# Kernel tuning notes

Hardware: AMD Instinct MI355X
Metric: run time of the kernel (lower is better)

The kernel has to match this reference:

```python
import jax, jax.numpy as jnp
import numpy as np


def setup_inputs() -> dict:
    key = jax.random.key(0)
    kq, kk, kv = jax.random.split(key, 3)
    B, T, D = 8, 4096, 64
    q = jax.random.normal(kq, (B, T, D), dtype=jnp.float32)
    k = jax.random.normal(kk, (B, T, D), dtype=jnp.float32)
    v = jax.random.normal(kv, (B, T, D), dtype=jnp.float32)
    return {"q": q, "k": k, "v": v}


def reference(q, k, v):
    # q,k,v: [b, t, d]
    b, t_q, d = q.shape
    t_k = k.shape[1]
    scale = 1.0 / jnp.sqrt(jnp.asarray(d, dtype=q.dtype))
    qk = jnp.einsum('bqd,bkd->bqk', q, k) * scale  # [b, t_q, t_k]
    # causal mask: positions t2 > t1 set to -inf (replaces the Python double-loop)
    causal_mask = jnp.arange(t_k)[None, :] > jnp.arange(t_q)[:, None]  # [t_q, t_k]
    qk = jnp.where(causal_mask[None, :, :], -jnp.inf, qk)
    attn = jax.nn.softmax(qk, axis=-1)
    return jnp.einsum('bqk,bkd->bqd', attn, v)
```

## Files before the change

### kernel.cpp

```cpp
#include <hip/hip_runtime.h>

namespace {

constexpr float QSC = 0.18033688f;

typedef short bf16x8 __attribute__((ext_vector_type(8)));
typedef float f32x4 __attribute__((ext_vector_type(4)));

typedef __attribute__((address_space(3))) unsigned int lds_u32;
typedef __attribute__((address_space(1))) const unsigned int gbl_u32;

__device__ inline float exp2x(float x) { return __builtin_amdgcn_exp2f(x); }

__device__ inline unsigned int pack2(float a, float b) {
  unsigned int ua = __builtin_bit_cast(unsigned int, a);
  unsigned int ub = __builtin_bit_cast(unsigned int, b);
  ua = (ua + 0x8000u) >> 16;
  ub = (ub + 0x8000u) & 0xFFFF0000u;
  return ua | ub;
}

__device__ inline void gl_lds16(const unsigned short* g, unsigned short* l) {
  __builtin_amdgcn_global_load_lds((gbl_u32*)g, (lds_u32*)l, 16, 0, 0);
}

__device__ inline bf16x8 ld16(const unsigned short* p) {
  uint4 u = *(const uint4*)p;
  return __builtin_bit_cast(bf16x8, u);
}

__global__ __launch_bounds__(256) void prep(const float* __restrict__ K,
                                            const float* __restrict__ V,
                                            unsigned short* __restrict__ Kbf,
                                            unsigned short* __restrict__ Vtb) {
  __shared__ float Vl[64 * 65];
  const int bid = blockIdx.x;
  const int b = bid >> 6, kt = bid & 63;
  const int tid = threadIdx.x;
  const float4* Ks4 = (const float4*)(K + ((size_t)b * 4096 + kt * 64) * 64);
  const float4* Vs4 = (const float4*)(V + ((size_t)b * 4096 + kt * 64) * 64);
  #pragma unroll
  for (int i = 0; i < 4; ++i) {
    int idx = tid + 256 * i;
    int row = idx >> 4, c4 = idx & 15;
    float4 t = Ks4[idx];
    *(uint2*)&Kbf[((size_t)b * 4096 + kt * 64 + row) * 64 + c4 * 4] =
        make_uint2(pack2(t.x, t.y), pack2(t.z, t.w));
    float4 tv = Vs4[idx];
    float* d = &Vl[row * 65 + c4 * 4];
    d[0] = tv.x; d[1] = tv.y; d[2] = tv.z; d[3] = tv.w;
  }
  __syncthreads();
  #pragma unroll
  for (int i = 0; i < 4; ++i) {
    int idx = tid + 256 * i;
    int dd = idx >> 4, kc = idx & 15;
    float a  = Vl[(kc * 4 + 0) * 65 + dd];
    float b2 = Vl[(kc * 4 + 1) * 65 + dd];
    float c  = Vl[(kc * 4 + 2) * 65 + dd];
    float e  = Vl[(kc * 4 + 3) * 65 + dd];
    *(uint2*)&Vtb[((size_t)b * 64 + dd) * 4096 + kt * 64 + kc * 4] =
        make_uint2(pack2(a, b2), pack2(c, e));
  }
}

__launch_bounds__(512, 4)
__global__ void fa_mfma(const float* __restrict__ Q,
                        float* __restrict__ O,
                        const unsigned short* __restrict__ Kbf,
                        const unsigned short* __restrict__ Vtb) {
  __shared__ __align__(16) unsigned short smem[32768];

  const int bid = blockIdx.x;
  int b, qt;
  if (bid < 256) { b = bid & 7; qt = bid >> 3; }
  else           { b = bid & 7; qt = 63 - ((bid - 256) >> 3); }

  const int tid  = threadIdx.x;
  const int w    = tid >> 6;
  const int g    = w >> 2;
  const int wg   = w & 3;
  const int lane = tid & 63;
  const int quad = lane >> 4;
  const int lc   = lane & 15;

  unsigned short* Kb0 = &smem[(g * 2 + 0) * 4096];
  unsigned short* Kb1 = &smem[(g * 2 + 1) * 4096];
  unsigned short* Vb  = &smem[16384 + g * 4096];
  unsigned short* Pl  = &smem[24576 + w * 1024];

  const unsigned short* Kt_g = Kbf + (size_t)b * 4096 * 64;
  const unsigned short* Vt_g = Vtb + (size_t)b * 64 * 4096;

  const int r0 = wg * 16 + (lane >> 3);
  const int c0 = (lane & 7) ^ (r0 & 7);

  const int ph0 = (quad ^ (lc & 7)) * 8;
  const int ph1 = ((4 + quad) ^ (lc & 7)) * 8;

  const size_t base = (size_t)b * 4096 * 64;
  const float* Qb = Q + base + (size_t)qt * 64 * 64;
  float* Ob = O + base + (size_t)qt * 64 * 64;

  bf16x8 qf[2];
  {
    const float* qrow = Qb + (wg * 16 + lc) * 64 + quad * 8;
    #pragma unroll
    for (int ks = 0; ks < 2; ++ks) {
      float4 x = *(const float4*)(qrow + ks * 32);
      float4 y = *(const float4*)(qrow + ks * 32 + 4);
      uint4 u = make_uint4(pack2(x.x * QSC, x.y * QSC), pack2(x.z * QSC, x.w * QSC),
                           pack2(y.x * QSC, y.y * QSC), pack2(y.z * QSC, y.w * QSC));
      qf[ks] = __builtin_bit_cast(bf16x8, u);
    }
  }

  if (g <= qt) {
    const unsigned short* gk = Kt_g + (size_t)(g * 64) * 64;
    gl_lds16(gk + (size_t)r0 * 64 + c0 * 8, Kb0 + wg * 1024);
    gl_lds16(gk + (size_t)(r0 + 8) * 64 + c0 * 8, Kb0 + wg * 1024 + 512);
  }

  float l_i = 0.0f;
  f32x4 o[4];
  #pragma unroll
  for (int nt = 0; nt < 4; ++nt) o[nt] = f32x4{0.f, 0.f, 0.f, 0.f};

  const int nIter = qt / 2 + 1;
  for (int i = 0; i < nIter; ++i) {
    const int kt = 2 * i + g;
    const bool active = (kt <= qt);
    unsigned short* Kcur = (i & 1) ? Kb1 : Kb0;
    unsigned short* Knxt = (i & 1) ? Kb0 : Kb1;

    __syncthreads();

    if (active) {
      const unsigned short* gv = Vt_g + kt * 64;
      gl_lds16(gv + (size_t)r0 * 4096 + c0 * 8, Vb + wg * 1024);
      gl_lds16(gv + (size_t)(r0 + 8) * 4096 + c0 * 8, Vb + wg * 1024 + 512);
    }
    if (kt + 2 <= qt) {
      const unsigned short* gk = Kt_g + (size_t)((kt + 2) * 64) * 64;
      gl_lds16(gk + (size_t)r0 * 64 + c0 * 8, Knxt + wg * 1024);
      gl_lds16(gk + (size_t)(r0 + 8) * 64 + c0 * 8, Knxt + wg * 1024 + 512);
    }

    if (active) {
      f32x4 st[4];
      #pragma unroll
      for (int t = 0; t < 4; ++t) {
        f32x4 c = {0.f, 0.f, 0.f, 0.f};
        c = __builtin_amdgcn_mfma_f32_16x16x32_bf16(ld16(&Kcur[(t * 16 + lc) * 64 + ph0]), qf[0], c, 0, 0, 0);
        c = __builtin_amdgcn_mfma_f32_16x16x32_bf16(ld16(&Kcur[(t * 16 + lc) * 64 + ph1]), qf[1], c, 0, 0, 0);
        st[t] = c;
      }

      const bool diag = (kt == qt);
      const int qrow = wg * 16 + lc;
      #pragma unroll
      for (int t = 0; t < 4; ++t) {
        float e[4];
        #pragma unroll
        for (int r = 0; r < 4; ++r) {
          int key_l = 16 * t + quad * 4 + r;
          float v = st[t][r];
          if (diag && key_l > qrow) v = -1e30f;
          e[r] = exp2x(v);
        }
        l_i += (e[0] + e[1]) + (e[2] + e[3]);
        *(uint2*)&Pl[lc * 64 + ((2 * t + (quad >> 1)) ^ (lc & 7)) * 8 + (quad & 1) * 4] =
            make_uint2(pack2(e[0], e[1]), pack2(e[2], e[3]));
      }
    }

    __syncthreads();

    if (active) {
      #pragma unroll
      for (int ks = 0; ks < 2; ++ks) {
        bf16x8 a = ld16(&Pl[lc * 64 + (ks ? ph1 : ph0)]);
        #pragma unroll
        for (int nt = 0; nt < 4; ++nt) {
          bf16x8 bfr = ld16(&Vb[(nt * 16 + lc) * 64 + (ks ? ph1 : ph0)]);
          o[nt] = __builtin_amdgcn_mfma_f32_16x16x32_bf16(a, bfr, o[nt], 0, 0, 0);
        }
      }
    }
  }

  l_i += __shfl_xor(l_i, 16);
  l_i += __shfl_xor(l_i, 32);

  constexpr int MSTR = 66;
  float* mrg = (float*)smem;
  if (g == 1) {
    #pragma unroll
    for (int r = 0; r < 4; ++r) {
      int row = wg * 16 + quad * 4 + r;
      #pragma unroll
      for (int nt = 0; nt < 4; ++nt)
        mrg[row * MSTR + nt * 16 + lc] = o[nt][r];
    }
    if (quad == 0)
      mrg[64 * MSTR + wg * 16 + lc] = l_i;
  }
  __syncthreads();
  if (g == 0) {
    const int row0 = wg * 16 + lc;
    float linv = 1.0f / (l_i + mrg[64 * MSTR + row0]);
    float lv[4];
    #pragma unroll
    for (int r = 0; r < 4; ++r) lv[r] = __shfl(linv, quad * 4 + r);
    #pragma unroll
    for (int r = 0; r < 4; ++r) {
      int row = wg * 16 + quad * 4 + r;
      float* orow = Ob + row * 64 + lc;
      #pragma unroll
      for (int nt = 0; nt < 4; ++nt) {
        float o1 = mrg[row * MSTR + nt * 16 + lc];
        orow[nt * 16] = (o[nt][r] + o1) * lv[r];
      }
    }
  }
}

}

extern "C" void kernel_launch(void* const* d_in, const int* in_sizes, int n_in,
                              void* d_out, int out_size, void* d_ws, size_t ws_size,
                              hipStream_t stream) {
  const float* q = (const float*)d_in[0];
  const float* k = (const float*)d_in[1];
  const float* v = (const float*)d_in[2];
  float* out = (float*)d_out;
  unsigned short* Kbf = (unsigned short*)d_ws;
  unsigned short* Vtb = Kbf + (size_t)8 * 4096 * 64;
  prep<<<dim3(512), dim3(256), 0, stream>>>(k, v, Kbf, Vtb);
  fa_mfma<<<dim3(512), dim3(512), 0, stream>>>(q, out, Kbf, Vtb);
}
```

Before: 121.0 us.

## Split KV halves across separate blocks with atomic-flag cross-block merge

Each query tile's two key-parity halves now run in separate 256-thread blocks (1024 blocks total) instead of two wave groups inside one 512-thread block. Partial outputs and row sums go to a global workspace, and the last-arriving block, found through an atomic counter, merges and normalizes them. The diagonal-mask branch is also split out so non-diagonal tiles skip the mask compare. The aim is finer scheduling granularity and lower per-block LDS, at the cost of extra global traffic, fences, and a bf16-rounded partial for the g=1 half.

Result: slower. 292.3 us (+141.6%).

```diff
diff --git a/kernel.cpp b/kernel.cpp
--- a/kernel.cpp
+++ b/kernel.cpp
@@ -20,6 +20,16 @@
   return ua | ub;
 }
 
+__device__ inline float bf2f(unsigned short u) {
+  unsigned int v = (unsigned int)u << 16;
+  return __builtin_bit_cast(float, v);
+}
+
+__device__ inline unsigned short f2bf(float a) {
+  unsigned int ua = __builtin_bit_cast(unsigned int, a);
+  return (unsigned short)((ua + 0x8000u) >> 16);
+}
+
 __device__ inline void gl_lds16(const unsigned short* g, unsigned short* l) {
   __builtin_amdgcn_global_load_lds((gbl_u32*)g, (lds_u32*)l, 16, 0, 0);
 }
@@ -32,11 +42,13 @@
 __global__ __launch_bounds__(256) void prep(const float* __restrict__ K,
                                             const float* __restrict__ V,
                                             unsigned short* __restrict__ Kbf,
-                                            unsigned short* __restrict__ Vtb) {
+                                            unsigned short* __restrict__ Vtb,
+                                            int* __restrict__ flags) {
   __shared__ float Vl[64 * 65];
   const int bid = blockIdx.x;
   const int b = bid >> 6, kt = bid & 63;
   const int tid = threadIdx.x;
+  if (tid == 0) flags[bid] = 0;
   const float4* Ks4 = (const float4*)(K + ((size_t)b * 4096 + kt * 64) * 64);
   const float4* Vs4 = (const float4*)(V + ((size_t)b * 4096 + kt * 64) * 64);
   #pragma unroll
@@ -64,35 +76,38 @@
   }
 }
 
-__launch_bounds__(512, 4)
+__launch_bounds__(256, 4)
 __global__ void fa_mfma(const float* __restrict__ Q,
                         float* __restrict__ O,
                         const unsigned short* __restrict__ Kbf,
-                        const unsigned short* __restrict__ Vtb) {
-  __shared__ __align__(16) unsigned short smem[32768];
+                        const unsigned short* __restrict__ Vtb,
+                        unsigned short* __restrict__ wsP,
+                        float* __restrict__ wsl,
+                        int* __restrict__ flags) {
+  __shared__ __align__(16) unsigned short smem[16384];
+  __shared__ int bcast;
 
   const int bid = blockIdx.x;
-  int b, qt;
-  if (bid < 256) { b = bid & 7; qt = bid >> 3; }
-  else           { b = bid & 7; qt = 63 - ((bid - 256) >> 3); }
+  const int j = bid & 255, s = bid >> 8;
+  const int b = j >> 5, a = j & 31;
+  const int qt = (s & 2) ? (63 - a) : a;
+  const int g = s & 1;
 
   const int tid  = threadIdx.x;
   const int w    = tid >> 6;
-  const int g    = w >> 2;
-  const int wg   = w & 3;
   const int lane = tid & 63;
   const int quad = lane >> 4;
   const int lc   = lane & 15;
 
-  unsigned short* Kb0 = &smem[(g * 2 + 0) * 4096];
-  unsigned short* Kb1 = &smem[(g * 2 + 1) * 4096];
-  unsigned short* Vb  = &smem[16384 + g * 4096];
-  unsigned short* Pl  = &smem[24576 + w * 1024];
+  unsigned short* Kb0 = &smem[0];
+  unsigned short* Kb1 = &smem[4096];
+  unsigned short* Vb  = &smem[8192];
+  unsigned short* Pl  = &smem[12288 + w * 1024];
 
   const unsigned short* Kt_g = Kbf + (size_t)b * 4096 * 64;
   const unsigned short* Vt_g = Vtb + (size_t)b * 64 * 4096;
 
-  const int r0 = wg * 16 + (lane >> 3);
+  const int r0 = w * 16 + (lane >> 3);
   const int c0 = (lane & 7) ^ (r0 & 7);
 
   const int ph0 = (quad ^ (lc & 7)) * 8;
@@ -101,10 +116,11 @@
   const size_t base = (size_t)b * 4096 * 64;
   const float* Qb = Q + base + (size_t)qt * 64 * 64;
   float* Ob = O + base + (size_t)qt * 64 * 64;
+  const int slot = b * 64 + qt;
 
   bf16x8 qf[2];
   {
-    const float* qrow = Qb + (wg * 16 + lc) * 64 + quad * 8;
+    const float* qrow = Qb + (w * 16 + lc) * 64 + quad * 8;
     #pragma unroll
     for (int ks = 0; ks < 2; ++ks) {
       float4 x = *(const float4*)(qrow + ks * 32);
@@ -117,8 +133,8 @@
 
   if (g <= qt) {
     const unsigned short* gk = Kt_g + (size_t)(g * 64) * 64;
-    gl_lds16(gk + (size_t)r0 * 64 + c0 * 8, Kb0 + wg * 1024);
-    gl_lds16(gk + (size_t)(r0 + 8) * 64 + c0 * 8, Kb0 + wg * 1024 + 512);
+    gl_lds16(gk + (size_t)r0 * 64 + c0 * 8, Kb0 + w * 1024);
+    gl_lds16(gk + (size_t)(r0 + 8) * 64 + c0 * 8, Kb0 + w * 1024 + 512);
   }
 
   float l_i = 0.0f;
@@ -137,13 +153,13 @@
 
     if (active) {
       const unsigned short* gv = Vt_g + kt * 64;
-      gl_lds16(gv + (size_t)r0 * 4096 + c0 * 8, Vb + wg * 1024);
-      gl_lds16(gv + (size_t)(r0 + 8) * 4096 + c0 * 8, Vb + wg * 1024 + 512);
+      gl_lds16(gv + (size_t)r0 * 4096 + c0 * 8, Vb + w * 1024);
+      gl_lds16(gv + (size_t)(r0 + 8) * 4096 + c0 * 8, Vb + w * 1024 + 512);
     }
     if (kt + 2 <= qt) {
       const unsigned short* gk = Kt_g + (size_t)((kt + 2) * 64) * 64;
-      gl_lds16(gk + (size_t)r0 * 64 + c0 * 8, Knxt + wg * 1024);
-      gl_lds16(gk + (size_t)(r0 + 8) * 64 + c0 * 8, Knxt + wg * 1024 + 512);
+      gl_lds16(gk + (size_t)r0 * 64 + c0 * 8, Knxt + w * 1024);
+      gl_lds16(gk + (size_t)(r0 + 8) * 64 + c0 * 8, Knxt + w * 1024 + 512);
     }
 
     if (active) {
@@ -156,21 +172,30 @@
         st[t] = c;
       }
 
-      const bool diag = (kt == qt);
-      const int qrow = wg * 16 + lc;
-      #pragma unroll
-      for (int t = 0; t < 4; ++t) {
-        float e[4];
+      if (kt == qt) {
+        const int qrow = w * 16 + lc;
         #pragma unroll
-        for (int r = 0; r < 4; ++r) {
-          int key_l = 16 * t + quad * 4 + r;
-          float v = st[t][r];
-          if (diag && key_l > qrow) v = -1e30f;
-          e[r] = exp2x(v);
+        for (int t = 0; t < 4; ++t) {
+          float e[4];
+          #pragma unroll
+          for (int r = 0; r < 4; ++r) {
+            int key_l = 16 * t + quad * 4 + r;
+            e[r] = (key_l > qrow) ? 0.0f : exp2x(st[t][r]);
+          }
+          l_i += (e[0] + e[1]) + (e[2] + e[3]);
+          *(uint2*)&Pl[lc * 64 + ((2 * t + (quad >> 1)) ^ (lc & 7)) * 8 + (quad & 1) * 4] =
+              make_uint2(pack2(e[0], e[1]), pack2(e[2], e[3]));
         }
-        l_i += (e[0] + e[1]) + (e[2] + e[3]);
-        *(uint2*)&Pl[lc * 64 + ((2 * t + (quad >> 1)) ^ (lc & 7)) * 8 + (quad & 1) * 4] =
-            make_uint2(pack2(e[0], e[1]), pack2(e[2], e[3]));
+      } else {
+        #pragma unroll
+        for (int t = 0; t < 4; ++t) {
+          float e[4];
+          #pragma unroll
+          for (int r = 0; r < 4; ++r) e[r] = exp2x(st[t][r]);
+          l_i += (e[0] + e[1]) + (e[2] + e[3]);
+          *(uint2*)&Pl[lc * 64 + ((2 * t + (quad >> 1)) ^ (lc & 7)) * 8 + (quad & 1) * 4] =
+              make_uint2(pack2(e[0], e[1]), pack2(e[2], e[3]));
+        }
       }
     }
 
@@ -179,11 +204,11 @@
     if (active) {
       #pragma unroll
       for (int ks = 0; ks < 2; ++ks) {
-        bf16x8 a = ld16(&Pl[lc * 64 + (ks ? ph1 : ph0)]);
+        bf16x8 pa = ld16(&Pl[lc * 64 + (ks ? ph1 : ph0)]);
         #pragma unroll
         for (int nt = 0; nt < 4; ++nt) {
           bf16x8 bfr = ld16(&Vb[(nt * 16 + lc) * 64 + (ks ? ph1 : ph0)]);
-          o[nt] = __builtin_amdgcn_mfma_f32_16x16x32_bf16(a, bfr, o[nt], 0, 0, 0);
+          o[nt] = __builtin_amdgcn_mfma_f32_16x16x32_bf16(pa, bfr, o[nt], 0, 0, 0);
         }
       }
     }
@@ -192,34 +217,41 @@
   l_i += __shfl_xor(l_i, 16);
   l_i += __shfl_xor(l_i, 32);
 
-  constexpr int MSTR = 66;
-  float* mrg = (float*)smem;
-  if (g == 1) {
+  if (g == 0) {
     #pragma unroll
     for (int r = 0; r < 4; ++r) {
-      int row = wg * 16 + quad * 4 + r;
-      #pragma unroll
-      for (int nt = 0; nt < 4; ++nt)
-        mrg[row * MSTR + nt * 16 + lc] = o[nt][r];
-    }
-    if (quad == 0)
-      mrg[64 * MSTR + wg * 16 + lc] = l_i;
-  }
+      int row = w * 16 + quad * 4 + r;
+      float* orow = Ob + row * 64 + lc;
+      #pragma unroll
+      for (int nt = 0; nt < 4; ++nt) orow[nt * 16] = o[nt][r];
+    }
+  } else {
+    unsigned short* ps = wsP + (size_t)slot * 4096;
+    #pragma unroll
+    for (int r = 0; r < 4; ++r) {
+      int row = w * 16 + quad * 4 + r;
+      #pragma unroll
+      for (int nt = 0; nt < 4; ++nt) ps[row * 64 + nt * 16 + lc] = f2bf(o[nt][r]);
+    }
+  }
+  if (quad == 0) wsl[slot * 128 + g * 64 + w * 16 + lc] = l_i;
+
+  __threadfence();
   __syncthreads();
-  if (g == 0) {
-    const int row0 = wg * 16 + lc;
-    float linv = 1.0f / (l_i + mrg[64 * MSTR + row0]);
-    float lv[4];
-    #pragma unroll
-    for (int r = 0; r < 4; ++r) lv[r] = __shfl(linv, quad * 4 + r);
+  if (tid == 0) bcast = atomicAdd(&flags[slot], 1);
+  __syncthreads();
+  if (bcast == 1) {
+    __threadfence();
+    const unsigned short* ps = wsP + (size_t)slot * 4096;
     #pragma unroll
     for (int r = 0; r < 4; ++r) {
-      int row = wg * 16 + quad * 4 + r;
+      int row = w * 16 + quad * 4 + r;
+      float linv = 1.0f / (wsl[slot * 128 + row] + wsl[slot * 128 + 64 + row]);
       float* orow = Ob + row * 64 + lc;
       #pragma unroll
       for (int nt = 0; nt < 4; ++nt) {
-        float o1 = mrg[row * MSTR + nt * 16 + lc];
-        orow[nt * 16] = (o[nt][r] + o1) * lv[r];
+        float sib = (g == 0) ? bf2f(ps[row * 64 + nt * 16 + lc]) : orow[nt * 16];
+        orow[nt * 16] = (o[nt][r] + sib) * linv;
       }
     }
   }
@@ -236,6 +268,9 @@
   float* out = (float*)d_out;
   unsigned short* Kbf = (unsigned short*)d_ws;
   unsigned short* Vtb = Kbf + (size_t)8 * 4096 * 64;
-  prep<<<dim3(512), dim3(256), 0, stream>>>(k, v, Kbf, Vtb);
-  fa_mfma<<<dim3(512), dim3(512), 0, stream>>>(q, out, Kbf, Vtb);
-}
+  unsigned short* wsP = Vtb + (size_t)8 * 4096 * 64;
+  float* wsl = (float*)(wsP + (size_t)512 * 4096);
+  int* flags = (int*)(wsl + (size_t)512 * 128);
+  prep<<<dim3(512), dim3(256), 0, stream>>>(k, v, Kbf, Vtb, flags);
+  fa_mfma<<<dim3(1024), dim3(256), 0, stream>>>(q, out, Kbf, Vtb, wsP, wsl, flags);
+}
```

## Load K and V fragments straight from global into registers, drop LDS staging

Applied to the files above, without the earlier changes.

Removes the double-buffered LDS staging of K and V tiles (global_load_lds) and the per-iteration block-wide barriers. Each wave now reads its MFMA operand fragments for K and transposed V directly from global memory into registers, and the masked diagonal tile gets its own softmax branch. This shrinks shared memory to the per-wave P scratch plus the merge area, which needs one barrier before the final merge. The cost is redundant global/L2 reads: the four waves in a group each fetch the same tiles. Load latency is also no longer hidden by a prefetch.

New measurement: 191.7 us. +58.5%, slower.

```diff
diff --git a/kernel.cpp b/kernel.cpp
--- a/kernel.cpp
+++ b/kernel.cpp
@@ -6,9 +6,6 @@
 
 typedef short bf16x8 __attribute__((ext_vector_type(8)));
 typedef float f32x4 __attribute__((ext_vector_type(4)));
-
-typedef __attribute__((address_space(3))) unsigned int lds_u32;
-typedef __attribute__((address_space(1))) const unsigned int gbl_u32;
 
 __device__ inline float exp2x(float x) { return __builtin_amdgcn_exp2f(x); }
 
@@ -18,10 +15,6 @@
   ua = (ua + 0x8000u) >> 16;
   ub = (ub + 0x8000u) & 0xFFFF0000u;
   return ua | ub;
-}
-
-__device__ inline void gl_lds16(const unsigned short* g, unsigned short* l) {
-  __builtin_amdgcn_global_load_lds((gbl_u32*)g, (lds_u32*)l, 16, 0, 0);
 }
 
 __device__ inline bf16x8 ld16(const unsigned short* p) {
@@ -69,7 +62,7 @@
                         float* __restrict__ O,
                         const unsigned short* __restrict__ Kbf,
                         const unsigned short* __restrict__ Vtb) {
-  __shared__ __align__(16) unsigned short smem[32768];
+  __shared__ __align__(16) unsigned short smem[8704];
 
   const int bid = blockIdx.x;
   int b, qt;
@@ -84,16 +77,10 @@
   const int quad = lane >> 4;
   const int lc   = lane & 15;
 
-  unsigned short* Kb0 = &smem[(g * 2 + 0) * 4096];
-  unsigned short* Kb1 = &smem[(g * 2 + 1) * 4096];
-  unsigned short* Vb  = &smem[16384 + g * 4096];
-  unsigned short* Pl  = &smem[24576 + w * 1024];
+  unsigned short* Pl = &smem[w * 1024];
 
   const unsigned short* Kt_g = Kbf + (size_t)b * 4096 * 64;
   const unsigned short* Vt_g = Vtb + (size_t)b * 64 * 4096;
-
-  const int r0 = wg * 16 + (lane >> 3);
-  const int c0 = (lane & 7) ^ (r0 & 7);
 
   const int ph0 = (quad ^ (lc & 7)) * 8;
   const int ph1 = ((4 + quad) ^ (lc & 7)) * 8;
@@ -115,48 +102,33 @@
     }
   }
 
-  if (g <= qt) {
-    const unsigned short* gk = Kt_g + (size_t)(g * 64) * 64;
-    gl_lds16(gk + (size_t)r0 * 64 + c0 * 8, Kb0 + wg * 1024);
-    gl_lds16(gk + (size_t)(r0 + 8) * 64 + c0 * 8, Kb0 + wg * 1024 + 512);
-  }
-
   float l_i = 0.0f;
   f32x4 o[4];
   #pragma unroll
   for (int nt = 0; nt < 4; ++nt) o[nt] = f32x4{0.f, 0.f, 0.f, 0.f};
 
-  const int nIter = qt / 2 + 1;
-  for (int i = 0; i < nIter; ++i) {
-    const int kt = 2 * i + g;
-    const bool active = (kt <= qt);
-    unsigned short* Kcur = (i & 1) ? Kb1 : Kb0;
-    unsigned short* Knxt = (i & 1) ? Kb0 : Kb1;
-
-    __syncthreads();
-
-    if (active) {
-      const unsigned short* gv = Vt_g + kt * 64;
-      gl_lds16(gv + (size_t)r0 * 4096 + c0 * 8, Vb + wg * 1024);
-      gl_lds16(gv + (size_t)(r0 + 8) * 4096 + c0 * 8, Vb + wg * 1024 + 512);
-    }
-    if (kt + 2 <= qt) {
-      const unsigned short* gk = Kt_g + (size_t)((kt + 2) * 64) * 64;
-      gl_lds16(gk + (size_t)r0 * 64 + c0 * 8, Knxt + wg * 1024);
-      gl_lds16(gk + (size_t)(r0 + 8) * 64 + c0 * 8, Knxt + wg * 1024 + 512);
-    }
-
-    if (active) {
-      f32x4 st[4];
-      #pragma unroll
-      for (int t = 0; t < 4; ++t) {
-        f32x4 c = {0.f, 0.f, 0.f, 0.f};
-        c = __builtin_amdgcn_mfma_f32_16x16x32_bf16(ld16(&Kcur[(t * 16 + lc) * 64 + ph0]), qf[0], c, 0, 0, 0);
-        c = __builtin_amdgcn_mfma_f32_16x16x32_bf16(ld16(&Kcur[(t * 16 + lc) * 64 + ph1]), qf[1], c, 0, 0, 0);
-        st[t] = c;
-      }
-
-      const bool diag = (kt == qt);
+  for (int kt = g; kt <= qt; kt += 2) {
+    const unsigned short* kb = Kt_g + (size_t)kt * 64 * 64;
+    f32x4 st[4];
+    #pragma unroll
+    for (int t = 0; t < 4; ++t) {
+      bf16x8 a0 = ld16(kb + (t * 16 + lc) * 64 + quad * 8);
+      bf16x8 a1 = ld16(kb + (t * 16 + lc) * 64 + 32 + quad * 8);
+      f32x4 c = {0.f, 0.f, 0.f, 0.f};
+      c = __builtin_amdgcn_mfma_f32_16x16x32_bf16(a0, qf[0], c, 0, 0, 0);
+      c = __builtin_amdgcn_mfma_f32_16x16x32_bf16(a1, qf[1], c, 0, 0, 0);
+      st[t] = c;
+    }
+
+    bf16x8 vf[4][2];
+    const unsigned short* vb = Vt_g + kt * 64;
+    #pragma unroll
+    for (int nt = 0; nt < 4; ++nt) {
+      vf[nt][0] = ld16(vb + (size_t)(nt * 16 + lc) * 4096 + quad * 8);
+      vf[nt][1] = ld16(vb + (size_t)(nt * 16 + lc) * 4096 + 32 + quad * 8);
+    }
+
+    if (kt == qt) {
       const int qrow = wg * 16 + lc;
       #pragma unroll
       for (int t = 0; t < 4; ++t) {
@@ -164,27 +136,31 @@
         #pragma unroll
         for (int r = 0; r < 4; ++r) {
           int key_l = 16 * t + quad * 4 + r;
-          float v = st[t][r];
-          if (diag && key_l > qrow) v = -1e30f;
-          e[r] = exp2x(v);
+          e[r] = (key_l > qrow) ? 0.0f : exp2x(st[t][r]);
         }
         l_i += (e[0] + e[1]) + (e[2] + e[3]);
         *(uint2*)&Pl[lc * 64 + ((2 * t + (quad >> 1)) ^ (lc & 7)) * 8 + (quad & 1) * 4] =
             make_uint2(pack2(e[0], e[1]), pack2(e[2], e[3]));
       }
-    }
-
-    __syncthreads();
-
-    if (active) {
-      #pragma unroll
-      for (int ks = 0; ks < 2; ++ks) {
-        bf16x8 a = ld16(&Pl[lc * 64 + (ks ? ph1 : ph0)]);
+    } else {
+      #pragma unroll
+      for (int t = 0; t < 4; ++t) {
+        float e[4];
         #pragma unroll
-        for (int nt = 0; nt < 4; ++nt) {
-          bf16x8 bfr = ld16(&Vb[(nt * 16 + lc) * 64 + (ks ? ph1 : ph0)]);
-          o[nt] = __builtin_amdgcn_mfma_f32_16x16x32_bf16(a, bfr, o[nt], 0, 0, 0);
-        }
+        for (int r = 0; r < 4; ++r) e[r] = exp2x(st[t][r]);
+        l_i += (e[0] + e[1]) + (e[2] + e[3]);
+        *(uint2*)&Pl[lc * 64 + ((2 * t + (quad >> 1)) ^ (lc & 7)) * 8 + (quad & 1) * 4] =
+            make_uint2(pack2(e[0], e[1]), pack2(e[2], e[3]));
+      }
+    }
+
+    {
+      bf16x8 pa0 = ld16(&Pl[lc * 64 + ph0]);
+      bf16x8 pa1 = ld16(&Pl[lc * 64 + ph1]);
+      #pragma unroll
+      for (int nt = 0; nt < 4; ++nt) {
+        o[nt] = __builtin_amdgcn_mfma_f32_16x16x32_bf16(pa0, vf[nt][0], o[nt], 0, 0, 0);
+        o[nt] = __builtin_amdgcn_mfma_f32_16x16x32_bf16(pa1, vf[nt][1], o[nt], 0, 0, 0);
       }
     }
   }
@@ -194,6 +170,7 @@
 
   constexpr int MSTR = 66;
   float* mrg = (float*)smem;
+  __syncthreads();
   if (g == 1) {
     #pragma unroll
     for (int r = 0; r < 4; ++r) {
```

## Split key and D halves across waves, read V fragments directly from global

Applied to the files above, without the earlier changes.

Reworks how work inside each 64x64 tile is split across the four waves of a group. Each wave now covers a 32-query by 32-key by 32-dim slice instead of 16 full query rows. The P tile is shared per group in LDS instead of being held per wave. V fragments are loaded straight from global into registers rather than staged through LDS, which shrinks LDS use and may raise occupancy. The cost is four partial accumulators that must be reduced through a serialized LDS merge with extra barriers, plus global-latency V loads inside the loop.

After: 121.2 us. About the same (+0.2%).

```diff
diff --git a/kernel.cpp b/kernel.cpp
--- a/kernel.cpp
+++ b/kernel.cpp
@@ -69,7 +69,7 @@
                         float* __restrict__ O,
                         const unsigned short* __restrict__ Kbf,
                         const unsigned short* __restrict__ Vtb) {
-  __shared__ __align__(16) unsigned short smem[32768];
+  __shared__ __align__(16) unsigned short smem[24576];
 
   const int bid = blockIdx.x;
   int b, qt;
@@ -80,14 +80,15 @@
   const int w    = tid >> 6;
   const int g    = w >> 2;
   const int wg   = w & 3;
+  const int kh   = wg & 1;
+  const int h2   = wg >> 1;
   const int lane = tid & 63;
   const int quad = lane >> 4;
   const int lc   = lane & 15;
 
   unsigned short* Kb0 = &smem[(g * 2 + 0) * 4096];
   unsigned short* Kb1 = &smem[(g * 2 + 1) * 4096];
-  unsigned short* Vb  = &smem[16384 + g * 4096];
-  unsigned short* Pl  = &smem[24576 + w * 1024];
+  unsigned short* Pg  = &smem[16384 + g * 4096];
 
   const unsigned short* Kt_g = Kbf + (size_t)b * 4096 * 64;
   const unsigned short* Vt_g = Vtb + (size_t)b * 64 * 4096;
@@ -95,23 +96,23 @@
   const int r0 = wg * 16 + (lane >> 3);
   const int c0 = (lane & 7) ^ (r0 & 7);
 
-  const int ph0 = (quad ^ (lc & 7)) * 8;
-  const int ph1 = ((4 + quad) ^ (lc & 7)) * 8;
+  const int lx = lc & 7;
 
   const size_t base = (size_t)b * 4096 * 64;
   const float* Qb = Q + base + (size_t)qt * 64 * 64;
   float* Ob = O + base + (size_t)qt * 64 * 64;
 
-  bf16x8 qf[2];
-  {
-    const float* qrow = Qb + (wg * 16 + lc) * 64 + quad * 8;
+  bf16x8 qf[2][2];
+  #pragma unroll
+  for (int q2 = 0; q2 < 2; ++q2) {
+    const float* qrow = Qb + (h2 * 32 + q2 * 16 + lc) * 64 + quad * 8;
     #pragma unroll
     for (int ks = 0; ks < 2; ++ks) {
       float4 x = *(const float4*)(qrow + ks * 32);
       float4 y = *(const float4*)(qrow + ks * 32 + 4);
       uint4 u = make_uint4(pack2(x.x * QSC, x.y * QSC), pack2(x.z * QSC, x.w * QSC),
                            pack2(y.x * QSC, y.y * QSC), pack2(y.z * QSC, y.w * QSC));
-      qf[ks] = __builtin_bit_cast(bf16x8, u);
+      qf[q2][ks] = __builtin_bit_cast(bf16x8, u);
     }
   }
 
@@ -121,10 +122,12 @@
     gl_lds16(gk + (size_t)(r0 + 8) * 64 + c0 * 8, Kb0 + wg * 1024 + 512);
   }
 
-  float l_i = 0.0f;
-  f32x4 o[4];
-  #pragma unroll
-  for (int nt = 0; nt < 4; ++nt) o[nt] = f32x4{0.f, 0.f, 0.f, 0.f};
+  float l_p[2] = {0.f, 0.f};
+  f32x4 o[4][2];
+  #pragma unroll
+  for (int m = 0; m < 4; ++m)
+    #pragma unroll
+    for (int n = 0; n < 2; ++n) o[m][n] = f32x4{0.f, 0.f, 0.f, 0.f};
 
   const int nIter = qt / 2 + 1;
   for (int i = 0; i < nIter; ++i) {
@@ -135,42 +138,50 @@
 
     __syncthreads();
 
-    if (active) {
-      const unsigned short* gv = Vt_g + kt * 64;
-      gl_lds16(gv + (size_t)r0 * 4096 + c0 * 8, Vb + wg * 1024);
-      gl_lds16(gv + (size_t)(r0 + 8) * 4096 + c0 * 8, Vb + wg * 1024 + 512);
-    }
     if (kt + 2 <= qt) {
       const unsigned short* gk = Kt_g + (size_t)((kt + 2) * 64) * 64;
       gl_lds16(gk + (size_t)r0 * 64 + c0 * 8, Knxt + wg * 1024);
       gl_lds16(gk + (size_t)(r0 + 8) * 64 + c0 * 8, Knxt + wg * 1024 + 512);
     }
 
+    bf16x8 vf[2];
     if (active) {
-      f32x4 st[4];
-      #pragma unroll
-      for (int t = 0; t < 4; ++t) {
-        f32x4 c = {0.f, 0.f, 0.f, 0.f};
-        c = __builtin_amdgcn_mfma_f32_16x16x32_bf16(ld16(&Kcur[(t * 16 + lc) * 64 + ph0]), qf[0], c, 0, 0, 0);
-        c = __builtin_amdgcn_mfma_f32_16x16x32_bf16(ld16(&Kcur[(t * 16 + lc) * 64 + ph1]), qf[1], c, 0, 0, 0);
-        st[t] = c;
+      #pragma unroll
+      for (int n = 0; n < 2; ++n)
+        vf[n] = ld16(Vt_g + (size_t)(h2 * 32 + n * 16 + lc) * 4096 + kt * 64 + kh * 32 + quad * 8);
+
+      f32x4 st[2][2];
+      #pragma unroll
+      for (int k2 = 0; k2 < 2; ++k2) {
+        const int arow = kh * 32 + k2 * 16 + lc;
+        bf16x8 a0 = ld16(Kcur + arow * 64 + (quad ^ lx) * 8);
+        bf16x8 a1 = ld16(Kcur + arow * 64 + ((4 + quad) ^ lx) * 8);
+        #pragma unroll
+        for (int q2 = 0; q2 < 2; ++q2) {
+          f32x4 c = {0.f, 0.f, 0.f, 0.f};
+          c = __builtin_amdgcn_mfma_f32_16x16x32_bf16(a0, qf[q2][0], c, 0, 0, 0);
+          c = __builtin_amdgcn_mfma_f32_16x16x32_bf16(a1, qf[q2][1], c, 0, 0, 0);
+          st[q2][k2] = c;
+        }
       }
 
       const bool diag = (kt == qt);
-      const int qrow = wg * 16 + lc;
-      #pragma unroll
-      for (int t = 0; t < 4; ++t) {
-        float e[4];
-        #pragma unroll
-        for (int r = 0; r < 4; ++r) {
-          int key_l = 16 * t + quad * 4 + r;
-          float v = st[t][r];
-          if (diag && key_l > qrow) v = -1e30f;
-          e[r] = exp2x(v);
-        }
-        l_i += (e[0] + e[1]) + (e[2] + e[3]);
-        *(uint2*)&Pl[lc * 64 + ((2 * t + (quad >> 1)) ^ (lc & 7)) * 8 + (quad & 1) * 4] =
-            make_uint2(pack2(e[0], e[1]), pack2(e[2], e[3]));
+      #pragma unroll
+      for (int q2 = 0; q2 < 2; ++q2) {
+        const int qrow_l = h2 * 32 + q2 * 16 + lc;
+        #pragma unroll
+        for (int k2 = 0; k2 < 2; ++k2) {
+          float e[4];
+          #pragma unroll
+          for (int r = 0; r < 4; ++r) {
+            int key_l = kh * 32 + k2 * 16 + quad * 4 + r;
+            float v = st[q2][k2][r];
+            e[r] = (diag && key_l > qrow_l) ? 0.0f : exp2x(v);
+          }
+          l_p[q2] += (e[0] + e[1]) + (e[2] + e[3]);
+          *(uint2*)&Pg[qrow_l * 64 + ((kh * 4 + k2 * 2 + (quad >> 1)) ^ lx) * 8 + (quad & 1) * 4] =
+              make_uint2(pack2(e[0], e[1]), pack2(e[2], e[3]));
+        }
       }
     }
 
@@ -178,50 +189,66 @@
 
     if (active) {
       #pragma unroll
-      for (int ks = 0; ks < 2; ++ks) {
-        bf16x8 a = ld16(&Pl[lc * 64 + (ks ? ph1 : ph0)]);
-        #pragma unroll
-        for (int nt = 0; nt < 4; ++nt) {
-          bf16x8 bfr = ld16(&Vb[(nt * 16 + lc) * 64 + (ks ? ph1 : ph0)]);
-          o[nt] = __builtin_amdgcn_mfma_f32_16x16x32_bf16(a, bfr, o[nt], 0, 0, 0);
-        }
-      }
-    }
-  }
-
-  l_i += __shfl_xor(l_i, 16);
-  l_i += __shfl_xor(l_i, 32);
-
-  constexpr int MSTR = 66;
+      for (int m = 0; m < 4; ++m) {
+        bf16x8 pa = ld16(&Pg[(m * 16 + lc) * 64 + ((kh * 4 + quad) ^ lx) * 8]);
+        #pragma unroll
+        for (int n = 0; n < 2; ++n)
+          o[m][n] = __builtin_amdgcn_mfma_f32_16x16x32_bf16(pa, vf[n], o[m][n], 0, 0, 0);
+      }
+    }
+  }
+
+  #pragma unroll
+  for (int q2 = 0; q2 < 2; ++q2) {
+    l_p[q2] += __shfl_xor(l_p[q2], 16);
+    l_p[q2] += __shfl_xor(l_p[q2], 32);
+  }
+
   float* mrg = (float*)smem;
-  if (g == 1) {
-    #pragma unroll
-    for (int r = 0; r < 4; ++r) {
-      int row = wg * 16 + quad * 4 + r;
-      #pragma unroll
-      for (int nt = 0; nt < 4; ++nt)
-        mrg[row * MSTR + nt * 16 + lc] = o[nt][r];
-    }
-    if (quad == 0)
-      mrg[64 * MSTR + wg * 16 + lc] = l_i;
-  }
-  __syncthreads();
-  if (g == 0) {
-    const int row0 = wg * 16 + lc;
-    float linv = 1.0f / (l_i + mrg[64 * MSTR + row0]);
-    float lv[4];
-    #pragma unroll
-    for (int r = 0; r < 4; ++r) lv[r] = __shfl(linv, quad * 4 + r);
-    #pragma unroll
-    for (int r = 0; r < 4; ++r) {
-      int row = wg * 16 + quad * 4 + r;
-      float* orow = Ob + row * 64 + lc;
-      #pragma unroll
-      for (int nt = 0; nt < 4; ++nt) {
-        float o1 = mrg[row * MSTR + nt * 16 + lc];
-        orow[nt * 16] = (o[nt][r] + o1) * lv[r];
-      }
-    }
+  float* l_lds = mrg + 2 * 64 * 33;
+  const int myset = g * 2 + kh;
+  for (int r = 0; r < 4; ++r) {
+    if (myset == r) {
+      float* md = mrg + h2 * (64 * 33);
+      if (r == 0) {
+        #pragma unroll
+        for (int m = 0; m < 4; ++m)
+          #pragma unroll
+          for (int n = 0; n < 2; ++n)
+            #pragma unroll
+            for (int e = 0; e < 4; ++e)
+              md[(m * 16 + quad * 4 + e) * 33 + n * 16 + lc] = o[m][n][e];
+        if (quad == 0) {
+          l_lds[h2 * 32 + lc] = l_p[0];
+          l_lds[h2 * 32 + 16 + lc] = l_p[1];
+        }
+      } else {
+        #pragma unroll
+        for (int m = 0; m < 4; ++m)
+          #pragma unroll
+          for (int n = 0; n < 2; ++n)
+            #pragma unroll
+            for (int e = 0; e < 4; ++e)
+              md[(m * 16 + quad * 4 + e) * 33 + n * 16 + lc] += o[m][n][e];
+        if (quad == 0) {
+          l_lds[h2 * 32 + lc] += l_p[0];
+          l_lds[h2 * 32 + 16 + lc] += l_p[1];
+        }
+      }
+    }
+    __syncthreads();
+  }
+
+  {
+    const int row = w * 8 + (lane >> 3);
+    const int cb = (lane & 7) * 8;
+    float linv = 1.0f / l_lds[row];
+    const float* mh = mrg + (cb >= 32 ? 64 * 33 : 0) + row * 33 + (cb & 31);
+    float4 v0, v1;
+    v0.x = mh[0] * linv; v0.y = mh[1] * linv; v0.z = mh[2] * linv; v0.w = mh[3] * linv;
+    v1.x = mh[4] * linv; v1.y = mh[5] * linv; v1.z = mh[6] * linv; v1.w = mh[7] * linv;
+    *(float4*)(Ob + row * 64 + cb) = v0;
+    *(float4*)(Ob + row * 64 + cb + 4) = v1;
   }
 }
 
```
